# Kernel optimization log

Measured on AMD Instinct MI355X. Metric: run time of the kernel, lower is better.

The kernel has to match this reference:

```python
import jax, jax.numpy as jnp
import numpy as np

N = 8192
E = 262144
C = 256          # in_channels
OUT = 256        # out_channels
H = 4            # num_heads
DH = C // H      # head dim


def setup_inputs() -> dict:
    key = jax.random.key(0)
    ks = jax.random.split(key, 12)
    stdv = 1.0 / np.sqrt(C)
    inp = {
        "x": jax.random.normal(ks[0], (N, C), dtype=jnp.float32),
        "adj": jax.random.randint(ks[1], (2, E), 0, N, dtype=jnp.int64),
        "weight_local": jax.random.uniform(ks[2], (C, C), jnp.float32, -stdv, stdv),
        # nn.MultiheadAttention packed projections
        "in_proj_w": jax.random.normal(ks[3], (3 * C, C), jnp.float32) * stdv,
        "in_proj_b": jnp.zeros((3 * C,), jnp.float32),
        "out_proj_w": jax.random.normal(ks[4], (C, C), jnp.float32) * stdv,
        "out_proj_b": jnp.zeros((C,), jnp.float32),
        "ln_g": jnp.ones((C,), jnp.float32),
        "ln_b": jnp.zeros((C,), jnp.float32),
        "alpha": jnp.zeros((), jnp.float32),
        "fc_w": jax.random.normal(ks[5], (OUT, C), jnp.float32) * stdv,
        "fc_b": jnp.zeros((OUT,), jnp.float32),
    }
    return inp


def _gcn_conv(x, edge_index):
    # out[col] += (1/sqrt(d[col]*d[row])) * x[row], d = in-degree by col
    row, col = edge_index[0], edge_index[1]
    n = x.shape[0]
    d = jax.ops.segment_sum(jnp.ones((edge_index.shape[1],), x.dtype), col, num_segments=n)
    val = jax.lax.rsqrt(d[col] * d[row])
    val = jnp.where(jnp.isfinite(val), val, 0.0)
    msg = x[row] * val[:, None]                      # [E, C] gather + scale
    return jax.ops.segment_sum(msg, col, num_segments=n)  # [N, C] scatter-add


def _mha(x, in_proj_w, in_proj_b, out_proj_w, out_proj_b):
    # single-batch self-attention over all N nodes
    qkv = x @ in_proj_w.T + in_proj_b                # [N, 3C]
    q, k, v = jnp.split(qkv, 3, axis=-1)
    def heads(t):
        return t.reshape(N, H, DH).transpose(1, 0, 2)  # [H, N, DH]
    q, k, v = heads(q), heads(k), heads(v)
    scores = jnp.einsum("hnd,hmd->hnm", q, k) / np.sqrt(DH)  # [H, N, N]
    attn = jax.nn.softmax(scores, axis=-1)
    out = jnp.einsum("hnm,hmd->hnd", attn, v)        # [H, N, DH]
    out = out.transpose(1, 0, 2).reshape(N, C)
    return out @ out_proj_w.T + out_proj_b


def _layernorm(x, g, b, eps=1e-5):
    mu = jnp.mean(x, axis=-1, keepdims=True)
    var = jnp.var(x, axis=-1, keepdims=True)
    return (x - mu) * jax.lax.rsqrt(var + eps) * g + b


def reference(x, adj, weight_local, in_proj_w, in_proj_b, out_proj_w, out_proj_b,
              ln_g, ln_b, alpha, fc_w, fc_b):
    hi = _gcn_conv(x, adj)
    local_embed = hi @ weight_local                   # [N, C]
    attn_out = _mha(x, in_proj_w, in_proj_b, out_proj_w, out_proj_b)
    global_embed = _layernorm(x + attn_out, ln_g, ln_b)
    w = jax.nn.sigmoid(alpha)
    combined = w * local_embed + (1.0 - w) * global_embed
    return combined @ fc_w.T + fc_b                   # [N, OUT]
```

## Files before the change

### kernel.cpp

```cpp
#include <hip/hip_runtime.h>
#include <hip/hip_bf16.h>
#include <math.h>

#define NN   8192
#define EE   262144
#define CC   256
#define HH   4

typedef __bf16 bf16;
typedef __bf16 bf16x8 __attribute__((ext_vector_type(8)));
typedef __bf16 bf16x4 __attribute__((ext_vector_type(4)));
typedef __bf16 bf16x2 __attribute__((ext_vector_type(2)));
typedef float  f32x4  __attribute__((ext_vector_type(4)));

static __device__ __forceinline__ bf16 f2bf(float f) { return (bf16)f; }

static __device__ __forceinline__ unsigned pk2(float a, float b) {
    __hip_bfloat162 h = __float22bfloat162_rn(float2{a, b});
    return *reinterpret_cast<unsigned*>(&h);
}

__global__ void prep_all(const float* __restrict__ x, bf16* __restrict__ xb,
                         const float* __restrict__ ipw, const float* __restrict__ opw,
                         const float* __restrict__ fcw, const float* __restrict__ wloc,
                         bf16* __restrict__ ipwb, bf16* __restrict__ opwb,
                         bf16* __restrict__ fcwb, bf16* __restrict__ wlTb,
                         const int* __restrict__ adj, int* __restrict__ ideg) {
    int b = blockIdx.x, t = threadIdx.x;
    if (b < 2048) {
        for (int i = b * 256 + t; i < NN * CC; i += 2048 * 256) xb[i] = f2bf(x[i]);
    } else if (b < 2816) { int i = (b - 2048) * 256 + t; ipwb[i] = f2bf(ipw[i]); }
    else if (b < 3072)   { int i = (b - 2816) * 256 + t; opwb[i] = f2bf(opw[i]); }
    else if (b < 3328)   { int i = (b - 3072) * 256 + t; fcwb[i] = f2bf(fcw[i]); }
    else if (b < 3584)   { int n = b - 3328;             wlTb[n * 256 + t] = f2bf(wloc[t * 256 + n]); }
    else {
        int e = (b - 3584) * 256 + t;
        if (e < EE) atomicAdd(&ideg[adj[EE + e]], 1);
    }
}

__global__ __launch_bounds__(256) void build_kv(const bf16* __restrict__ qkv,
                                                bf16* __restrict__ Kpk,
                                                bf16* __restrict__ Vpk) {
    __shared__ bf16 tl[64][72];
    const int bx = blockIdx.x;
    const int h  = blockIdx.y;
    const int tid = threadIdx.x;
    #pragma unroll
    for (int i = 0; i < 2; i++) {
        int u = tid + i * 256;
        int key = u >> 3, g = u & 7;
        *reinterpret_cast<bf16x8*>(&tl[key][g * 8]) =
            *reinterpret_cast<const bf16x8*>(qkv + (size_t)(bx * 64 + key) * 768 + 256 + h * 64 + g * 8);
    }
    __syncthreads();
    #pragma unroll
    for (int i = 0; i < 2; i++) {
        int ee = tid + i * 256;
        int l15 = ee & 15, quad = (ee >> 4) & 3, c = (ee >> 6) & 1, ktl = ee >> 7;
        int key_local = (ktl >> 1) * 32 + (l15 >> 2) * 8 + (ktl & 1) * 4 + (l15 & 3);
        bf16x8 v = *reinterpret_cast<const bf16x8*>(&tl[key_local][c * 32 + quad * 8]);
        *reinterpret_cast<bf16x8*>(Kpk + ((size_t)((h * 512 + bx * 4 + ktl) * 2 + c)) * 512
                                       + (quad * 16 + l15) * 8) = v;
    }
    __syncthreads();
    #pragma unroll
    for (int i = 0; i < 2; i++) {
        int u = tid + i * 256;
        int key = u >> 3, g = u & 7;
        *reinterpret_cast<bf16x8*>(&tl[key][g * 8]) =
            *reinterpret_cast<const bf16x8*>(qkv + (size_t)(bx * 64 + key) * 768 + 512 + h * 64 + g * 8);
    }
    __syncthreads();
    #pragma unroll
    for (int i = 0; i < 2; i++) {
        int ee = tid + i * 256;
        int l15 = ee & 15, quad = (ee >> 4) & 3, nt = (ee >> 6) & 3, kcl = ee >> 8;
        bf16x8 v;
        #pragma unroll
        for (int j = 0; j < 8; j++) v[j] = tl[kcl * 32 + quad * 8 + j][nt * 16 + l15];
        *reinterpret_cast<bf16x8*>(Vpk + ((size_t)((h * 256 + bx * 2 + kcl) * 4 + nt)) * 512
                                       + (quad * 16 + l15) * 8) = v;
    }
}

__global__ __launch_bounds__(256) void scan_offsets(const int* __restrict__ ideg,
        int* __restrict__ off, int* __restrict__ cursor, float* __restrict__ rs) {
    __shared__ int ps[256];
    const int tid = threadIdx.x;
    const int base = tid * 32;
    int loc[32];
    int s = 0;
    #pragma unroll
    for (int i = 0; i < 32; i++) { loc[i] = s; s += ideg[base + i]; }
    ps[tid] = s;
    __syncthreads();
    for (int d = 1; d < 256; d <<= 1) {
        int v = (tid >= d) ? ps[tid - d] : 0;
        __syncthreads();
        ps[tid] += v;
        __syncthreads();
    }
    int excl = ps[tid] - s;
    #pragma unroll
    for (int i = 0; i < 32; i++) {
        int o = excl + loc[i];
        off[base + i] = o;
        cursor[base + i] = o;
        int dg = ideg[base + i];
        rs[base + i] = dg > 0 ? rsqrtf((float)dg) : 0.f;
    }
    if (tid == 255) off[8192] = excl + s;
}

__global__ void fill_csr(const int* __restrict__ adj, int* __restrict__ cursor,
                         int* __restrict__ csr) {
    int e = blockIdx.x * 256 + threadIdx.x;
    if (e < EE) {
        int col = adj[EE + e];
        int pos = atomicAdd(&cursor[col], 1);
        csr[pos] = adj[e];
    }
}

__global__ __launch_bounds__(256) void gemm_bt(
        const bf16* __restrict__ A, const bf16* __restrict__ W,
        const float* __restrict__ bias,
        float* __restrict__ outF, bf16* __restrict__ outB,
        int M, int N, int K) {
    const int tid  = threadIdx.x;
    const int wave = tid >> 6;
    const int lane = tid & 63;
    const int quad = lane >> 4;
    const int l15  = lane & 15;
    const int m0 = blockIdx.x * 128;
    const int n0 = blockIdx.y * 64;

    __shared__ bf16 Alds[128][72];
    __shared__ bf16 Wlds[64][72];

    f32x4 acc[2][4];
    #pragma unroll
    for (int mt = 0; mt < 2; mt++)
        #pragma unroll
        for (int nt = 0; nt < 4; nt++)
            acc[mt][nt] = (f32x4){0.f, 0.f, 0.f, 0.f};

    for (int k0 = 0; k0 < K; k0 += 64) {
        #pragma unroll
        for (int i = 0; i < 4; i++) {
            int u = tid + i * 256;
            int r = u >> 3;
            int cp = u & 7;
            *reinterpret_cast<bf16x8*>(&Alds[r][cp * 8]) =
                *reinterpret_cast<const bf16x8*>(A + (size_t)(m0 + r) * K + k0 + cp * 8);
        }
        #pragma unroll
        for (int i = 0; i < 2; i++) {
            int u = tid + i * 256;
            int r = u >> 3;
            int cp = u & 7;
            *reinterpret_cast<bf16x8*>(&Wlds[r][cp * 8]) =
                *reinterpret_cast<const bf16x8*>(W + (size_t)(n0 + r) * K + k0 + cp * 8);
        }
        __syncthreads();
        #pragma unroll
        for (int c = 0; c < 2; c++) {
            bf16x8 af[2], wf[4];
            #pragma unroll
            for (int mt = 0; mt < 2; mt++)
                af[mt] = *reinterpret_cast<const bf16x8*>(&Alds[wave * 32 + mt * 16 + l15][c * 32 + quad * 8]);
            #pragma unroll
            for (int nt = 0; nt < 4; nt++)
                wf[nt] = *reinterpret_cast<const bf16x8*>(&Wlds[nt * 16 + l15][c * 32 + quad * 8]);
            #pragma unroll
            for (int mt = 0; mt < 2; mt++)
                #pragma unroll
                for (int nt = 0; nt < 4; nt++)
                    acc[mt][nt] = __builtin_amdgcn_mfma_f32_16x16x32_bf16(af[mt], wf[nt], acc[mt][nt], 0, 0, 0);
        }
        __syncthreads();
    }
    #pragma unroll
    for (int mt = 0; mt < 2; mt++)
        #pragma unroll
        for (int nt = 0; nt < 4; nt++)
            #pragma unroll
            for (int r = 0; r < 4; r++) {
                int m = m0 + wave * 32 + mt * 16 + quad * 4 + r;
                int n = n0 + nt * 16 + l15;
                float v = acc[mt][nt][r];
                if (bias) v += bias[n];
                if (outF) outF[(size_t)m * N + n] = v;
                else      outB[(size_t)m * N + n] = f2bf(v);
            }
}

__global__ __launch_bounds__(512, 2) void flash_gather(const bf16* __restrict__ qkv,
                                                       const bf16* __restrict__ Kpk,
                                                       const bf16* __restrict__ Vpk,
                                                       bf16* __restrict__ attnO,
                                                       const bf16* __restrict__ xb,
                                                       const int* __restrict__ csr,
                                                       const int* __restrict__ off,
                                                       const float* __restrict__ rs,
                                                       bf16* __restrict__ hib) {
    __shared__ bf16 Osh[8][64][68];
    __shared__ float lsh[8][64];

    if (blockIdx.x >= 256) {
        const int gb = blockIdx.x - 256;
        const int grp = threadIdx.x >> 7;
        const int j = threadIdx.x & 127;
        #pragma unroll
        for (int round = 0; round < 4; round++) {
            const int col = gb * 4 + grp + round * 2048;
            const int o = off[col];
            const int cnt = off[col + 1] - o;
            const float rsc = rs[col];
            float a0 = 0.f, a1 = 0.f;
            int e = 0;
            for (; e + 4 <= cnt; e += 4) {
                int r0 = csr[o + e], r1 = csr[o + e + 1], r2 = csr[o + e + 2], r3 = csr[o + e + 3];
                float v0 = rsc * rs[r0], v1 = rsc * rs[r1], v2 = rsc * rs[r2], v3 = rsc * rs[r3];
                unsigned u0 = ((const unsigned*)(xb + (size_t)r0 * CC))[j];
                unsigned u1 = ((const unsigned*)(xb + (size_t)r1 * CC))[j];
                unsigned u2 = ((const unsigned*)(xb + (size_t)r2 * CC))[j];
                unsigned u3 = ((const unsigned*)(xb + (size_t)r3 * CC))[j];
                a0 += __uint_as_float(u0 << 16) * v0 + __uint_as_float(u1 << 16) * v1
                    + __uint_as_float(u2 << 16) * v2 + __uint_as_float(u3 << 16) * v3;
                a1 += __uint_as_float(u0 & 0xffff0000u) * v0 + __uint_as_float(u1 & 0xffff0000u) * v1
                    + __uint_as_float(u2 & 0xffff0000u) * v2 + __uint_as_float(u3 & 0xffff0000u) * v3;
            }
            for (; e < cnt; e++) {
                int r0 = csr[o + e];
                float v0 = rsc * rs[r0];
                unsigned u0 = ((const unsigned*)(xb + (size_t)r0 * CC))[j];
                a0 += __uint_as_float(u0 << 16) * v0;
                a1 += __uint_as_float(u0 & 0xffff0000u) * v0;
            }
            bf16x2 pk; pk[0] = f2bf(a0); pk[1] = f2bf(a1);
            ((bf16x2*)(hib + (size_t)col * CC))[j] = pk;
        }
        return;
    }

    const int tid  = threadIdx.x;
    const int w    = tid >> 6;
    const int g    = w >> 2;
    const int k4   = w & 3;
    const int lane = tid & 63;
    const int quad = lane >> 4;
    const int l15  = lane & 15;
    const int bx = blockIdx.x;
    const int h  = bx & 3;
    const int qb = bx >> 2;
    const int qbase = qb * 128 + g * 64;

    const float qs = 0.180336880f;
    bf16x8 qf[4][2];
    #pragma unroll
    for (int qt = 0; qt < 4; qt++)
        #pragma unroll
        for (int c = 0; c < 2; c++) {
            bf16x8 raw = *reinterpret_cast<const bf16x8*>(
                qkv + (size_t)(qbase + qt * 16 + l15) * 768 + h * 64 + c * 32 + quad * 8);
            #pragma unroll
            for (int j = 0; j < 8; j++) qf[qt][c][j] = f2bf((float)raw[j] * qs);
        }

    const bf16* Kb = Kpk + (size_t)h * 524288 + lane * 8;
    const bf16* Vb = Vpk + (size_t)h * 524288 + lane * 8;

    f32x4 oacc[4][4];
    #pragma unroll
    for (int qt = 0; qt < 4; qt++)
        #pragma unroll
        for (int nt = 0; nt < 4; nt++) oacc[qt][nt] = (f32x4){0.f, 0.f, 0.f, 0.f};
    f32x4 lacc[4];
    #pragma unroll
    for (int qt = 0; qt < 4; qt++) lacc[qt] = (f32x4){0.f, 0.f, 0.f, 0.f};
    bf16x8 onesf;
    #pragma unroll
    for (int j = 0; j < 8; j++) onesf[j] = f2bf(1.0f);
    const f32x4 z4 = (f32x4){0.f, 0.f, 0.f, 0.f};

    bf16x8 kfA[2][2], vfA[4], kfB[2][2], vfB[4];

    #define LOADKV(kc, kf, vf)                                                          \
        {                                                                               \
            _Pragma("unroll")                                                           \
            for (int s = 0; s < 2; s++)                                                 \
                _Pragma("unroll")                                                       \
                for (int c = 0; c < 2; c++)                                             \
                    kf[s][c] = *reinterpret_cast<const bf16x8*>(Kb + (kc) * 2048 + s * 1024 + c * 512); \
            _Pragma("unroll")                                                           \
            for (int nt = 0; nt < 4; nt++)                                              \
                vf[nt] = *reinterpret_cast<const bf16x8*>(Vb + (kc) * 2048 + nt * 512); \
        }

    #define COMPUTE(kf, vf)                                                             \
        {                                                                               \
            f32x4 sacc[2][4];                                                           \
            _Pragma("unroll")                                                           \
            for (int s = 0; s < 2; s++)                                                 \
                _Pragma("unroll")                                                       \
                for (int qt = 0; qt < 4; qt++) {                                        \
                    sacc[s][qt] = __builtin_amdgcn_mfma_f32_16x16x32_bf16(kf[s][0], qf[qt][0], z4, 0, 0, 0); \
                    sacc[s][qt] = __builtin_amdgcn_mfma_f32_16x16x32_bf16(kf[s][1], qf[qt][1], sacc[s][qt], 0, 0, 0); \
                }                                                                       \
            _Pragma("unroll")                                                           \
            for (int qt = 0; qt < 4; qt++) {                                            \
                float e0 = __builtin_amdgcn_exp2f(sacc[0][qt][0]);                      \
                float e1 = __builtin_amdgcn_exp2f(sacc[0][qt][1]);                      \
                float e2 = __builtin_amdgcn_exp2f(sacc[0][qt][2]);                      \
                float e3 = __builtin_amdgcn_exp2f(sacc[0][qt][3]);                      \
                float e4 = __builtin_amdgcn_exp2f(sacc[1][qt][0]);                      \
                float e5 = __builtin_amdgcn_exp2f(sacc[1][qt][1]);                      \
                float e6 = __builtin_amdgcn_exp2f(sacc[1][qt][2]);                      \
                float e7 = __builtin_amdgcn_exp2f(sacc[1][qt][3]);                      \
                union { bf16x8 v; unsigned u[4]; } pu;                                  \
                pu.u[0] = pk2(e0, e1);                                                  \
                pu.u[1] = pk2(e2, e3);                                                  \
                pu.u[2] = pk2(e4, e5);                                                  \
                pu.u[3] = pk2(e6, e7);                                                  \
                _Pragma("unroll")                                                       \
                for (int nt = 0; nt < 4; nt++)                                          \
                    oacc[qt][nt] = __builtin_amdgcn_mfma_f32_16x16x32_bf16(pu.v, vf[nt], oacc[qt][nt], 0, 0, 0); \
                lacc[qt] = __builtin_amdgcn_mfma_f32_16x16x32_bf16(pu.v, onesf, lacc[qt], 0, 0, 0); \
            }                                                                           \
        }

    LOADKV(k4, kfA, vfA);
    for (int it = 0; it < 64; it += 2) {
        const int kB = k4 + (it + 1) * 4;
        LOADKV(kB, kfB, vfB);
        COMPUTE(kfA, vfA);
        int kA2 = k4 + (it + 2) * 4;
        if (kA2 > 255) kA2 = k4;
        LOADKV(kA2, kfA, vfA);
        COMPUTE(kfB, vfB);
    }
    #undef LOADKV
    #undef COMPUTE

    #pragma unroll
    for (int qt = 0; qt < 4; qt++)
        #pragma unroll
        for (int nt = 0; nt < 4; nt++)
            #pragma unroll
            for (int r = 0; r < 4; r++)
                Osh[w][qt * 16 + quad * 4 + r][nt * 16 + l15] = f2bf(oacc[qt][nt][r]);
    if (l15 == 0) {
        #pragma unroll
        for (int qt = 0; qt < 4; qt++)
            #pragma unroll
            for (int r = 0; r < 4; r++)
                lsh[w][qt * 16 + quad * 4 + r] = lacc[qt][r];
    }
    __syncthreads();

    const int q7 = tid >> 2;
    const int gg = q7 >> 6;
    const int ql = q7 & 63;
    const int ds = (tid & 3) * 16;
    const int wb = gg * 4;
    float lsum = lsh[wb][ql] + lsh[wb + 1][ql] + lsh[wb + 2][ql] + lsh[wb + 3][ql];
    float linv = 1.f / lsum;
    float acc[16];
    #pragma unroll
    for (int i = 0; i < 16; i++) acc[i] = 0.f;
    #pragma unroll
    for (int v = 0; v < 4; v++) {
        bf16x8 o0 = *reinterpret_cast<const bf16x8*>(&Osh[wb + v][ql][ds]);
        bf16x8 o1 = *reinterpret_cast<const bf16x8*>(&Osh[wb + v][ql][ds + 8]);
        #pragma unroll
        for (int i = 0; i < 8; i++) { acc[i] += (float)o0[i]; acc[8 + i] += (float)o1[i]; }
    }
    bf16x8 ob0, ob1;
    #pragma unroll
    for (int i = 0; i < 8; i++) {
        ob0[i] = f2bf(acc[i] * linv);
        ob1[i] = f2bf(acc[8 + i] * linv);
    }
    bf16* dst = attnO + (size_t)(qb * 128 + q7) * CC + h * 64 + ds;
    *reinterpret_cast<bf16x8*>(dst) = ob0;
    *reinterpret_cast<bf16x8*>(dst + 8) = ob1;
}

__global__ __launch_bounds__(256) void gemm_ln_fc(
        const bf16* __restrict__ aOb, const bf16* __restrict__ opwb, const float* __restrict__ opb,
        const bf16* __restrict__ hib, const bf16* __restrict__ wlTb,
        const float* __restrict__ x, const float* __restrict__ lng, const float* __restrict__ lnb,
        const float* __restrict__ alp, const bf16* __restrict__ fcwb, const float* __restrict__ fcb,
        float* __restrict__ out) {
    const int tid = threadIdx.x;
    const int w = tid >> 6, lane = tid & 63, quad = lane >> 4, l15 = lane & 15;
    const int m0 = blockIdx.x * 16;
    const int n0w = w * 64;
    const f32x4 z4 = (f32x4){0.f, 0.f, 0.f, 0.f};

    __shared__ bf16 Ab[16][264];
    __shared__ float Xl[16][260];
    __shared__ float rsum[4][16], rsq[4][16];

    #pragma unroll
    for (int i = 0; i < 4; i++) {
        int u = tid + i * 256;
        int row = u >> 6, cp = (u & 63) * 4;
        *reinterpret_cast<f32x4*>(&Xl[row][cp]) =
            *reinterpret_cast<const f32x4*>(x + (size_t)(m0 + row) * CC + cp);
    }

    #pragma unroll
    for (int i = 0; i < 2; i++) {
        int u = tid + i * 256;
        int row = u >> 5, cp = (u & 31) * 8;
        *reinterpret_cast<bf16x8*>(&Ab[row][cp]) =
            *reinterpret_cast<const bf16x8*>(aOb + (size_t)(m0 + row) * CC + cp);
    }
    __syncthreads();
    f32x4 r0[4], r1[4], acc[4];
    #pragma unroll
    for (int nt = 0; nt < 4; nt++) acc[nt] = z4;
    for (int kc = 0; kc < 4; kc++)
        #pragma unroll
        for (int c = 0; c < 2; c++) {
            bf16x8 af = *reinterpret_cast<const bf16x8*>(&Ab[l15][kc * 64 + c * 32 + quad * 8]);
            #pragma unroll
            for (int nt = 0; nt < 4; nt++) {
                bf16x8 wf = *reinterpret_cast<const bf16x8*>(
                    opwb + (size_t)(n0w + nt * 16 + l15) * CC + kc * 64 + c * 32 + quad * 8);
                acc[nt] = __builtin_amdgcn_mfma_f32_16x16x32_bf16(af, wf, acc[nt], 0, 0, 0);
            }
        }
    #pragma unroll
    for (int nt = 0; nt < 4; nt++) r0[nt] = acc[nt];
    __syncthreads();

    #pragma unroll
    for (int i = 0; i < 2; i++) {
        int u = tid + i * 256;
        int row = u >> 5, cp = (u & 31) * 8;
        *reinterpret_cast<bf16x8*>(&Ab[row][cp]) =
            *reinterpret_cast<const bf16x8*>(hib + (size_t)(m0 + row) * CC + cp);
    }
    __syncthreads();
    #pragma unroll
    for (int nt = 0; nt < 4; nt++) acc[nt] = z4;
    for (int kc = 0; kc < 4; kc++)
        #pragma unroll
        for (int c = 0; c < 2; c++) {
            bf16x8 af = *reinterpret_cast<const bf16x8*>(&Ab[l15][kc * 64 + c * 32 + quad * 8]);
            #pragma unroll
            for (int nt = 0; nt < 4; nt++) {
                bf16x8 wf = *reinterpret_cast<const bf16x8*>(
                    wlTb + (size_t)(n0w + nt * 16 + l15) * CC + kc * 64 + c * 32 + quad * 8);
                acc[nt] = __builtin_amdgcn_mfma_f32_16x16x32_bf16(af, wf, acc[nt], 0, 0, 0);
            }
        }
    #pragma unroll
    for (int nt = 0; nt < 4; nt++) r1[nt] = acc[nt];
    __syncthreads();

    float v[4][4];
    #pragma unroll
    for (int nt = 0; nt < 4; nt++) {
        float bias0 = opb[n0w + nt * 16 + l15];
        #pragma unroll
        for (int r = 0; r < 4; r++)
            v[nt][r] = Xl[quad * 4 + r][n0w + nt * 16 + l15] + r0[nt][r] + bias0;
    }
    #pragma unroll
    for (int r = 0; r < 4; r++) {
        float s = v[0][r] + v[1][r] + v[2][r] + v[3][r];
        float s2 = v[0][r] * v[0][r] + v[1][r] * v[1][r] + v[2][r] * v[2][r] + v[3][r] * v[3][r];
        #pragma unroll
        for (int o = 1; o < 16; o <<= 1) { s += __shfl_xor(s, o); s2 += __shfl_xor(s2, o); }
        if (l15 == 0) { rsum[w][quad * 4 + r] = s; rsq[w][quad * 4 + r] = s2; }
    }
    __syncthreads();

    const float wgt = 1.f / (1.f + __expf(-alp[0]));
    float gv[4], bv[4], fb[4];
    #pragma unroll
    for (int nt = 0; nt < 4; nt++) {
        int n = n0w + nt * 16 + l15;
        gv[nt] = lng[n]; bv[nt] = lnb[n]; fb[nt] = fcb[n];
    }
    #pragma unroll
    for (int r = 0; r < 4; r++) {
        int row = quad * 4 + r;
        float S = rsum[0][row] + rsum[1][row] + rsum[2][row] + rsum[3][row];
        float S2 = rsq[0][row] + rsq[1][row] + rsq[2][row] + rsq[3][row];
        float mu = S * (1.f / CC);
        float var = S2 * (1.f / CC) - mu * mu;
        float rstd = rsqrtf(var + 1e-5f);
        #pragma unroll
        for (int nt = 0; nt < 4; nt++) {
            float ln = (v[nt][r] - mu) * rstd * gv[nt] + bv[nt];
            float cmb = wgt * r1[nt][r] + (1.f - wgt) * ln;
            Ab[row][n0w + nt * 16 + l15] = f2bf(cmb);
        }
    }
    __syncthreads();

    #pragma unroll
    for (int nt = 0; nt < 4; nt++) acc[nt] = z4;
    for (int kc = 0; kc < 4; kc++)
        #pragma unroll
        for (int c = 0; c < 2; c++) {
            bf16x8 af = *reinterpret_cast<const bf16x8*>(&Ab[l15][kc * 64 + c * 32 + quad * 8]);
            #pragma unroll
            for (int nt = 0; nt < 4; nt++) {
                bf16x8 wf = *reinterpret_cast<const bf16x8*>(
                    fcwb + (size_t)(n0w + nt * 16 + l15) * CC + kc * 64 + c * 32 + quad * 8);
                acc[nt] = __builtin_amdgcn_mfma_f32_16x16x32_bf16(af, wf, acc[nt], 0, 0, 0);
            }
        }
    #pragma unroll
    for (int nt = 0; nt < 4; nt++)
        #pragma unroll
        for (int r = 0; r < 4; r++)
            out[(size_t)(m0 + quad * 4 + r) * CC + n0w + nt * 16 + l15] = acc[nt][r] + fb[nt];
}

extern "C" void kernel_launch(void* const* d_in, const int* in_sizes, int n_in,
                              void* d_out, int out_size, void* d_ws, size_t ws_size,
                              hipStream_t stream) {
    (void)in_sizes; (void)n_in; (void)out_size; (void)ws_size;
    const float* x    = (const float*)d_in[0];
    const int*   adj  = (const int*)d_in[1];
    const float* wloc = (const float*)d_in[2];
    const float* ipw  = (const float*)d_in[3];
    const float* ipb  = (const float*)d_in[4];
    const float* opw  = (const float*)d_in[5];
    const float* opb  = (const float*)d_in[6];
    const float* lng  = (const float*)d_in[7];
    const float* lnb  = (const float*)d_in[8];
    const float* alp  = (const float*)d_in[9];
    const float* fcw  = (const float*)d_in[10];
    const float* fcb  = (const float*)d_in[11];
    float* out = (float*)d_out;

    char* p = (char*)d_ws;
    int*   ideg   = (int*)p;    p += (size_t)NN * 4;
    int*   off    = (int*)p;    p += (size_t)(NN + 1) * 4;
    int*   cursor = (int*)p;    p += (size_t)NN * 4;
    float* rs     = (float*)p;  p += (size_t)NN * 4;
    int*   csr    = (int*)p;    p += (size_t)EE * 4;
    bf16* xb    = (bf16*)p;   p += (size_t)NN * CC * 2;
    bf16* hib   = (bf16*)p;   p += (size_t)NN * CC * 2;
    bf16* ipwb  = (bf16*)p;   p += (size_t)768 * 256 * 2;
    bf16* wlTb  = (bf16*)p;   p += (size_t)256 * 256 * 2;
    bf16* opwb  = (bf16*)p;   p += (size_t)256 * 256 * 2;
    bf16* fcwb  = (bf16*)p;   p += (size_t)256 * 256 * 2;
    bf16* qkvb  = (bf16*)p;   p += (size_t)NN * 768 * 2;
    bf16* Kpk   = (bf16*)p;   p += (size_t)HH * 512 * 2 * 512 * 2;
    bf16* Vpk   = (bf16*)p;   p += (size_t)HH * 256 * 4 * 512 * 2;
    bf16* aOb   = (bf16*)p;   p += (size_t)NN * CC * 2;

    hipMemsetAsync(ideg, 0, (size_t)NN * 4, stream);

    prep_all<<<4608, 256, 0, stream>>>(x, xb, ipw, opw, fcw, wloc, ipwb, opwb, fcwb, wlTb, adj, ideg);
    scan_offsets<<<1, 256, 0, stream>>>(ideg, off, cursor, rs);
    fill_csr<<<EE / 256, 256, 0, stream>>>(adj, cursor, csr);

    gemm_bt<<<dim3(NN / 128, 768 / 64), 256, 0, stream>>>(xb, ipwb, ipb, nullptr, qkvb, NN, 768, 256);
    build_kv<<<dim3(NN / 64, HH), 256, 0, stream>>>(qkvb, Kpk, Vpk);
    flash_gather<<<768, 512, 0, stream>>>(qkvb, Kpk, Vpk, aOb, xb, csr, off, rs, hib);
    gemm_ln_fc<<<NN / 16, 256, 0, stream>>>(aOb, opwb, opb, hib, wlTb, x, lng, lnb, alp, fcwb, fcb, out);
}
```

Measured before the change: 276.6 us.

## Split GCN gather out of flash attention into a dedicated kernel

Moves the GCN neighbor gather out of the extra blocks of the fused flash-attention kernel and into a standalone kernel launched right after CSR construction. Each block handles two nodes with an 8-way unrolled gather, and the attention kernel now launches only its 256 attention blocks. This removes the co-scheduling of gather blocks alongside attention blocks, which may have shared resources or caused imbalance. In exchange the gather no longer overlaps with attention and costs an extra launch.

```diff
diff --git a/kernel.cpp b/kernel.cpp
--- a/kernel.cpp
+++ b/kernel.cpp
@@ -123,6 +123,46 @@
     }
 }
 
+__global__ __launch_bounds__(256) void gcn_gather3(const bf16* __restrict__ xb,
+        const int* __restrict__ csr, const int* __restrict__ off,
+        const float* __restrict__ rs, bf16* __restrict__ hib) {
+    const int node = blockIdx.x * 2 + (threadIdx.x >> 7);
+    const int j = threadIdx.x & 127;
+    const int o = off[node];
+    const int cnt = off[node + 1] - o;
+    const float rsc = rs[node];
+    const unsigned* xrow = (const unsigned*)xb;
+    float a0 = 0.f, a1 = 0.f;
+    int e = 0;
+    for (; e + 8 <= cnt; e += 8) {
+        int r[8];
+        float v[8];
+        unsigned u[8];
+        #pragma unroll
+        for (int i = 0; i < 8; i++) r[i] = csr[o + e + i];
+        #pragma unroll
+        for (int i = 0; i < 8; i++) v[i] = rsc * rs[r[i]];
+        #pragma unroll
+        for (int i = 0; i < 8; i++) u[i] = xrow[(size_t)r[i] * 128 + j];
+        #pragma unroll
+        for (int i = 0; i < 8; i++) {
+            a0 += __uint_as_float(u[i] << 16) * v[i];
+            a1 += __uint_as_float(u[i] & 0xffff0000u) * v[i];
+        }
+    }
+    for (; e < cnt; e++) {
+        int r0 = csr[o + e];
+        float v0 = rsc * rs[r0];
+        unsigned u0 = xrow[(size_t)r0 * 128 + j];
+        a0 += __uint_as_float(u0 << 16) * v0;
+        a1 += __uint_as_float(u0 & 0xffff0000u) * v0;
+    }
+    bf16x2 pk;
+    pk[0] = f2bf(a0);
+    pk[1] = f2bf(a1);
+    ((bf16x2*)(hib + (size_t)node * CC))[j] = pk;
+}
+
 __global__ __launch_bounds__(256) void gemm_bt(
         const bf16* __restrict__ A, const bf16* __restrict__ W,
         const float* __restrict__ bias,
@@ -196,55 +236,10 @@
             }
 }
 
-__global__ __launch_bounds__(512, 2) void flash_gather(const bf16* __restrict__ qkv,
+__global__ __launch_bounds__(512, 2) void flash_attn10(const bf16* __restrict__ qkv,
                                                        const bf16* __restrict__ Kpk,
                                                        const bf16* __restrict__ Vpk,
-                                                       bf16* __restrict__ attnO,
-                                                       const bf16* __restrict__ xb,
-                                                       const int* __restrict__ csr,
-                                                       const int* __restrict__ off,
-                                                       const float* __restrict__ rs,
-                                                       bf16* __restrict__ hib) {
-    __shared__ bf16 Osh[8][64][68];
-    __shared__ float lsh[8][64];
-
-    if (blockIdx.x >= 256) {
-        const int gb = blockIdx.x - 256;
-        const int grp = threadIdx.x >> 7;
-        const int j = threadIdx.x & 127;
-        #pragma unroll
-        for (int round = 0; round < 4; round++) {
-            const int col = gb * 4 + grp + round * 2048;
-            const int o = off[col];
-            const int cnt = off[col + 1] - o;
-            const float rsc = rs[col];
-            float a0 = 0.f, a1 = 0.f;
-            int e = 0;
-            for (; e + 4 <= cnt; e += 4) {
-                int r0 = csr[o + e], r1 = csr[o + e + 1], r2 = csr[o + e + 2], r3 = csr[o + e + 3];
-                float v0 = rsc * rs[r0], v1 = rsc * rs[r1], v2 = rsc * rs[r2], v3 = rsc * rs[r3];
-                unsigned u0 = ((const unsigned*)(xb + (size_t)r0 * CC))[j];
-                unsigned u1 = ((const unsigned*)(xb + (size_t)r1 * CC))[j];
-                unsigned u2 = ((const unsigned*)(xb + (size_t)r2 * CC))[j];
-                unsigned u3 = ((const unsigned*)(xb + (size_t)r3 * CC))[j];
-                a0 += __uint_as_float(u0 << 16) * v0 + __uint_as_float(u1 << 16) * v1
-                    + __uint_as_float(u2 << 16) * v2 + __uint_as_float(u3 << 16) * v3;
-                a1 += __uint_as_float(u0 & 0xffff0000u) * v0 + __uint_as_float(u1 & 0xffff0000u) * v1
-                    + __uint_as_float(u2 & 0xffff0000u) * v2 + __uint_as_float(u3 & 0xffff0000u) * v3;
-            }
-            for (; e < cnt; e++) {
-                int r0 = csr[o + e];
-                float v0 = rsc * rs[r0];
-                unsigned u0 = ((const unsigned*)(xb + (size_t)r0 * CC))[j];
-                a0 += __uint_as_float(u0 << 16) * v0;
-                a1 += __uint_as_float(u0 & 0xffff0000u) * v0;
-            }
-            bf16x2 pk; pk[0] = f2bf(a0); pk[1] = f2bf(a1);
-            ((bf16x2*)(hib + (size_t)col * CC))[j] = pk;
-        }
-        return;
-    }
-
+                                                       bf16* __restrict__ attnO) {
     const int tid  = threadIdx.x;
     const int w    = tid >> 6;
     const int g    = w >> 2;
@@ -256,6 +251,9 @@
     const int h  = bx & 3;
     const int qb = bx >> 2;
     const int qbase = qb * 128 + g * 64;
+
+    __shared__ bf16 Osh[8][64][68];
+    __shared__ float lsh[8][64];
 
     const float qs = 0.180336880f;
     bf16x8 qf[4][2];
@@ -565,9 +563,10 @@
     prep_all<<<4608, 256, 0, stream>>>(x, xb, ipw, opw, fcw, wloc, ipwb, opwb, fcwb, wlTb, adj, ideg);
     scan_offsets<<<1, 256, 0, stream>>>(ideg, off, cursor, rs);
     fill_csr<<<EE / 256, 256, 0, stream>>>(adj, cursor, csr);
+    gcn_gather3<<<NN / 2, 256, 0, stream>>>(xb, csr, off, rs, hib);
 
     gemm_bt<<<dim3(NN / 128, 768 / 64), 256, 0, stream>>>(xb, ipwb, ipb, nullptr, qkvb, NN, 768, 256);
     build_kv<<<dim3(NN / 64, HH), 256, 0, stream>>>(qkvb, Kpk, Vpk);
-    flash_gather<<<768, 512, 0, stream>>>(qkvb, Kpk, Vpk, aOb, xb, csr, off, rs, hib);
+    flash_attn10<<<256, 512, 0, stream>>>(qkvb, Kpk, Vpk, aOb);
     gemm_ln_fc<<<NN / 16, 256, 0, stream>>>(aOb, opwb, opb, hib, wlTb, x, lng, lnb, alp, fcwb, fcb, out);
 }
```

Result: faster. 255.2 us (-7.7%).
